# Kernel optimization log

Measured on AMD Instinct MI355X. Metric: run time of the kernel, lower is better.

## Reference

```python
import jax, jax.numpy as jnp
import numpy as np

S, B_BOX, C = 7, 2, 20
LAMBDA_COORD = 5.0
LAMBDA_NOOBJ = 0.5


def _iou(b1, b2):
    # b1, b2: [..., 4] in (cx, cy, w, h) format
    area1 = b1[..., 2] * b1[..., 3]
    area2 = b2[..., 2] * b2[..., 3]
    max_left = jnp.maximum(b1[..., 0] - b1[..., 2] / 2, b2[..., 0] - b2[..., 2] / 2)
    min_right = jnp.minimum(b1[..., 0] + b1[..., 2] / 2, b2[..., 0] + b2[..., 2] / 2)
    max_top = jnp.maximum(b1[..., 1] - b1[..., 3] / 2, b2[..., 1] - b2[..., 3] / 2)
    min_bottom = jnp.minimum(b1[..., 1] + b1[..., 3] / 2, b2[..., 1] + b2[..., 3] / 2)
    iw = jnp.maximum(min_right - max_left, 0.0)
    ih = jnp.maximum(min_bottom - max_top, 0.0)
    inter = iw * ih
    union = area1 + area2 - inter
    return jnp.where(inter > 0.0, inter / union, 0.0)


def setup_inputs() -> dict:
    key = jax.random.key(0)
    k1, k2, k3 = jax.random.split(key, 3)
    batch = 16384
    shape = (batch, S, S, C + 5 * B_BOX)  # [..., 30]
    pred = jax.random.uniform(k1, shape, dtype=jnp.float32)
    target = jax.random.uniform(k2, shape, dtype=jnp.float32)
    # objectness flag must be exactly 1.0 to trigger the obj branch
    obj_flag = jax.random.bernoulli(k3, 0.3, shape[:-1]).astype(jnp.float32)
    target = target.at[..., 0].set(obj_flag)
    return {"pred": pred, "target": target}


def reference(pred, target):
    batch = pred.shape[0]
    pred = pred.reshape(-1, S, S, C + 5 * B_BOX)
    target = target.reshape(-1, S, S, C + 5 * B_BOX)

    obj = (target[..., 0] == 1.0)          # [b,S,S] bool
    obj_f = obj.astype(pred.dtype)
    noobj_f = 1.0 - obj_f

    gt = target[..., 1:5]
    box1 = pred[..., 1:5]                   # predictor 1 box
    box2 = target[..., 6:10]                # NOTE: original code uses target's 2nd box
    iou1 = jax.lax.stop_gradient(_iou(box1, gt))
    iou2 = jax.lax.stop_gradient(_iou(box2, gt))
    resp1 = iou1 > iou2                     # predictor 1 responsible (strict >)
    r1 = resp1[..., None]

    # coord losses (responsible predictor)
    pxy = jnp.where(r1, pred[..., 1:3], pred[..., 6:8])
    txy = jnp.where(r1, target[..., 1:3], target[..., 6:8])
    pwh = jnp.where(r1, pred[..., 3:5], pred[..., 8:10])
    twh = jnp.where(r1, target[..., 3:5], target[..., 8:10])
    cell_xy = jnp.sum((pxy - txy) ** 2, axis=-1)
    cell_wh = jnp.sum((jnp.sqrt(pwh) - jnp.sqrt(twh)) ** 2, axis=-1)

    # obj confidence loss: responsible conf vs its iou
    conf_resp = jnp.where(resp1, pred[..., 0], pred[..., 5])
    iou_resp = jnp.where(resp1, iou1, iou2)
    cell_obj = (conf_resp - iou_resp) ** 2

    # noobj: non-responsible conf in obj cells; both confs in empty cells
    conf_other = jnp.where(resp1, pred[..., 5], pred[..., 0])
    cell_noobj_obj = conf_other ** 2
    cell_noobj_empty = pred[..., 0] ** 2 + pred[..., 5] ** 2

    cell_class = jnp.sum((pred[..., 10:] - target[..., 10:]) ** 2, axis=-1)

    loss_coord_xy = LAMBDA_COORD * jnp.sum(obj_f * cell_xy)
    loss_coord_wh = LAMBDA_COORD * jnp.sum(obj_f * cell_wh)
    loss_obj = jnp.sum(obj_f * cell_obj)
    loss_noobj = LAMBDA_NOOBJ * (jnp.sum(obj_f * cell_noobj_obj) + jnp.sum(noobj_f * cell_noobj_empty))
    loss_class = jnp.sum(obj_f * cell_class)
    loss = loss_coord_xy + loss_coord_wh + loss_obj + loss_noobj + loss_class

    bs = jnp.asarray(batch, pred.dtype)
    return ((loss_coord_xy + loss_coord_wh) / bs,
            loss_obj / bs,
            loss_noobj / bs,
            loss_class / bs,
            loss / bs)
```

## Files before the change

kernel.cpp:

```cpp
#include <hip/hip_runtime.h>

#define NCH 30
#define F2PC 15
#define F4PP 15
#define THREADS 256

typedef float fvec2 __attribute__((ext_vector_type(2)));
typedef float fvec4 __attribute__((ext_vector_type(4)));

__device__ __forceinline__ float iou_fn(float x1, float y1, float w1, float h1,
                                        float x2, float y2, float w2, float h2) {
    float a1 = w1 * h1, a2 = w2 * h2;
    float left  = fmaxf(x1 - w1 * 0.5f, x2 - w2 * 0.5f);
    float right = fminf(x1 + w1 * 0.5f, x2 + w2 * 0.5f);
    float top   = fmaxf(y1 - h1 * 0.5f, y2 - h2 * 0.5f);
    float bot   = fminf(y1 + h1 * 0.5f, y2 + h2 * 0.5f);
    float iw = fmaxf(right - left, 0.0f);
    float ih = fmaxf(bot - top, 0.0f);
    float inter = iw * ih;
    float uni = a1 + a2 - inter;
    return (inter > 0.0f) ? (inter / uni) : 0.0f;
}

__device__ __forceinline__ void cell_losses(const float* p, const float* t,
                                            float& coord, float& lobj,
                                            float& lnoobj, float& lclass) {
    float obj_f = (t[0] == 1.0f) ? 1.0f : 0.0f;

    float iou1 = iou_fn(p[1], p[2], p[3], p[4], t[1], t[2], t[3], t[4]);
    float iou2 = iou_fn(t[6], t[7], t[8], t[9], t[1], t[2], t[3], t[4]);
    bool r = iou1 > iou2;

    float px = r ? p[1] : p[6], py = r ? p[2] : p[7];
    float pw = r ? p[3] : p[8], ph = r ? p[4] : p[9];
    float tx = r ? t[1] : t[6], ty = r ? t[2] : t[7];
    float tw = r ? t[3] : t[8], th = r ? t[4] : t[9];

    float dx = px - tx, dy = py - ty;
    float cxy = dx * dx + dy * dy;
    float swv = sqrtf(pw) - sqrtf(tw), shv = sqrtf(ph) - sqrtf(th);
    float cwh = swv * swv + shv * shv;

    float conf_resp  = r ? p[0] : p[5];
    float iou_resp   = r ? iou1 : iou2;
    float conf_other = r ? p[5] : p[0];
    float dconf = conf_resp - iou_resp;

    coord  += obj_f * (cxy + cwh);
    lobj   += obj_f * dconf * dconf;
    lnoobj += obj_f * conf_other * conf_other
            + (1.0f - obj_f) * (p[0] * p[0] + p[5] * p[5]);

    float cls = 0.0f;
#pragma unroll
    for (int i = 10; i < NCH; i++) { float e = p[i] - t[i]; cls += e * e; }
    lclass += obj_f * cls;
}

__global__ __launch_bounds__(THREADS) void yolo_main(
        const fvec4* __restrict__ pred4, const fvec4* __restrict__ targ4,
        float4* __restrict__ partials, int n_pairs, int n_cells) {
    const int tid = threadIdx.x;
    float coord = 0.f, lobj = 0.f, lnoobj = 0.f, lclass = 0.f;

    for (long long i = (long long)blockIdx.x * THREADS + tid;
         i < n_pairs;
         i += (long long)gridDim.x * THREADS) {
        const long long c0 = 2 * i;
        if (c0 + 1 < (long long)n_cells) {
            float p[2 * NCH], t[2 * NCH];
            const fvec4* pp = pred4 + i * F4PP;
            const fvec4* tp = targ4 + i * F4PP;
#pragma unroll
            for (int k = 0; k < F4PP; k++) {
                fvec4 v = pp[k];
                p[4 * k] = v.x; p[4 * k + 1] = v.y; p[4 * k + 2] = v.z; p[4 * k + 3] = v.w;
            }
#pragma unroll
            for (int k = 0; k < F4PP; k++) {
                fvec4 v = tp[k];
                t[4 * k] = v.x; t[4 * k + 1] = v.y; t[4 * k + 2] = v.z; t[4 * k + 3] = v.w;
            }
            cell_losses(p, t, coord, lobj, lnoobj, lclass);
            cell_losses(p + NCH, t + NCH, coord, lobj, lnoobj, lclass);
        } else if (c0 < (long long)n_cells) {
            float p[NCH], t[NCH];
            const fvec2* pp = reinterpret_cast<const fvec2*>(pred4) + c0 * F2PC;
            const fvec2* tp = reinterpret_cast<const fvec2*>(targ4) + c0 * F2PC;
#pragma unroll
            for (int k = 0; k < F2PC; k++) { fvec2 v = pp[k]; p[2 * k] = v.x; p[2 * k + 1] = v.y; }
#pragma unroll
            for (int k = 0; k < F2PC; k++) { fvec2 v = tp[k]; t[2 * k] = v.x; t[2 * k + 1] = v.y; }
            cell_losses(p, t, coord, lobj, lnoobj, lclass);
        }
    }

#pragma unroll
    for (int off = 32; off > 0; off >>= 1) {
        coord  += __shfl_down(coord, off);
        lobj   += __shfl_down(lobj, off);
        lnoobj += __shfl_down(lnoobj, off);
        lclass += __shfl_down(lclass, off);
    }

    __shared__ float red[4][4];
    int lane = tid & 63;
    int wid  = tid >> 6;
    if (lane == 0) {
        red[wid][0] = coord; red[wid][1] = lobj;
        red[wid][2] = lnoobj; red[wid][3] = lclass;
    }
    __syncthreads();
    if (tid == 0) {
        float s0 = 0.f, s1 = 0.f, s2 = 0.f, s3 = 0.f;
        for (int w = 0; w < 4; w++) {
            s0 += red[w][0]; s1 += red[w][1];
            s2 += red[w][2]; s3 += red[w][3];
        }
        partials[blockIdx.x] = make_float4(s0, s1, s2, s3);
    }
}

__global__ __launch_bounds__(THREADS) void yolo_reduce(
        const float4* __restrict__ partials, int nparts,
        float* __restrict__ out, double inv_bs) {
    double s0 = 0.0, s1 = 0.0, s2 = 0.0, s3 = 0.0;
    for (int i = threadIdx.x; i < nparts; i += THREADS) {
        float4 v = partials[i];
        s0 += (double)v.x; s1 += (double)v.y;
        s2 += (double)v.z; s3 += (double)v.w;
    }
#pragma unroll
    for (int off = 32; off > 0; off >>= 1) {
        s0 += __shfl_down(s0, off);
        s1 += __shfl_down(s1, off);
        s2 += __shfl_down(s2, off);
        s3 += __shfl_down(s3, off);
    }
    __shared__ double red[4][4];
    int lane = threadIdx.x & 63;
    int wid  = threadIdx.x >> 6;
    if (lane == 0) {
        red[wid][0] = s0; red[wid][1] = s1;
        red[wid][2] = s2; red[wid][3] = s3;
    }
    __syncthreads();
    if (threadIdx.x == 0) {
        double a0 = 0, a1 = 0, a2 = 0, a3 = 0;
        for (int w = 0; w < 4; w++) {
            a0 += red[w][0]; a1 += red[w][1];
            a2 += red[w][2]; a3 += red[w][3];
        }
        double cd = a0 * 5.0 * inv_bs;
        double o  = a1 * inv_bs;
        double n  = a2 * 0.5 * inv_bs;
        double cl = a3 * inv_bs;
        out[0] = (float)cd;
        out[1] = (float)o;
        out[2] = (float)n;
        out[3] = (float)cl;
        out[4] = (float)(cd + o + n + cl);
    }
}

extern "C" void kernel_launch(void* const* d_in, const int* in_sizes, int n_in,
                              void* d_out, int out_size, void* d_ws, size_t ws_size,
                              hipStream_t stream) {
    const fvec4* pred4 = (const fvec4*)d_in[0];
    const fvec4* targ4 = (const fvec4*)d_in[1];
    float* out = (float*)d_out;
    float4* partials = (float4*)d_ws;

    int n_cells = in_sizes[0] / NCH;
    int batch   = n_cells / 49;
    int n_pairs = (n_cells + 1) / 2;

    int grid = (n_pairs + THREADS - 1) / THREADS;
    if (grid < 1) grid = 1;

    int max_parts = (int)(ws_size / sizeof(float4));
    if (max_parts >= 1 && grid > max_parts) grid = max_parts;

    yolo_main<<<grid, THREADS, 0, stream>>>(pred4, targ4, partials, n_pairs, n_cells);
    yolo_reduce<<<1, THREADS, 0, stream>>>(partials, grid, out, 1.0 / (double)batch);
}
```

Before: 212.1 us.

## Stage cell tiles through LDS with coalesced loads and register prefetch

Each 64-thread block now loads a 64-cell tile with fully coalesced float4 loads into registers. It writes the tile to LDS, and each thread then reads its own cell from there. This replaces the old strided per-thread float4 loads. The next tile is prefetched into registers while the current one is computed, and the grid is capped so blocks loop persistently. This targets uncoalesced global access; the cost is LDS traffic and bank conflicts from the stride-15 fvec2 reads, plus small one-wave blocks.

```diff
diff --git a/kernel.cpp b/kernel.cpp
--- a/kernel.cpp
+++ b/kernel.cpp
@@ -2,8 +2,9 @@
 
 #define NCH 30
 #define F2PC 15
-#define F4PP 15
-#define THREADS 256
+#define TILE 64
+#define TPB 64
+#define MAXB 2560
 
 typedef float fvec2 __attribute__((ext_vector_type(2)));
 typedef float fvec4 __attribute__((ext_vector_type(4)));
@@ -57,41 +58,81 @@
     lclass += obj_f * cls;
 }
 
-__global__ __launch_bounds__(THREADS) void yolo_main(
-        const fvec4* __restrict__ pred4, const fvec4* __restrict__ targ4,
-        float4* __restrict__ partials, int n_pairs, int n_cells) {
-    const int tid = threadIdx.x;
+__global__ __launch_bounds__(TPB) void yolo_main(
+        const float* __restrict__ pred, const float* __restrict__ targ,
+        float4* __restrict__ partials, int n_full, int n_cells) {
+    __shared__ fvec4 sp4[TILE * F2PC / 2];
+    __shared__ fvec4 st4[TILE * F2PC / 2];
+
+    const int lane = threadIdx.x;
     float coord = 0.f, lobj = 0.f, lnoobj = 0.f, lclass = 0.f;
 
-    for (long long i = (long long)blockIdx.x * THREADS + tid;
-         i < n_pairs;
-         i += (long long)gridDim.x * THREADS) {
-        const long long c0 = 2 * i;
-        if (c0 + 1 < (long long)n_cells) {
-            float p[2 * NCH], t[2 * NCH];
-            const fvec4* pp = pred4 + i * F4PP;
-            const fvec4* tp = targ4 + i * F4PP;
-#pragma unroll
-            for (int k = 0; k < F4PP; k++) {
-                fvec4 v = pp[k];
-                p[4 * k] = v.x; p[4 * k + 1] = v.y; p[4 * k + 2] = v.z; p[4 * k + 3] = v.w;
+    fvec4 rp[7], rt[7];
+    fvec2 rp7, rt7;
+
+    int t = blockIdx.x;
+    bool have = t < n_full;
+    if (have) {
+        const long long b4 = (long long)t * 480;
+#pragma unroll
+        for (int k = 0; k < 7; k++) {
+            rp[k] = reinterpret_cast<const fvec4*>(pred)[b4 + k * 64 + lane];
+            rt[k] = reinterpret_cast<const fvec4*>(targ)[b4 + k * 64 + lane];
+        }
+        rp7 = reinterpret_cast<const fvec2*>(pred)[2 * b4 + 896 + lane];
+        rt7 = reinterpret_cast<const fvec2*>(targ)[2 * b4 + 896 + lane];
+    }
+
+    while (have) {
+        const int tn = t + gridDim.x;
+        const bool have_n = tn < n_full;
+
+        __syncthreads();
+#pragma unroll
+        for (int k = 0; k < 7; k++) {
+            sp4[k * 64 + lane] = rp[k];
+            st4[k * 64 + lane] = rt[k];
+        }
+        reinterpret_cast<fvec2*>(sp4)[896 + lane] = rp7;
+        reinterpret_cast<fvec2*>(st4)[896 + lane] = rt7;
+        __syncthreads();
+
+        if (have_n) {
+            const long long b4 = (long long)tn * 480;
+#pragma unroll
+            for (int k = 0; k < 7; k++) {
+                rp[k] = reinterpret_cast<const fvec4*>(pred)[b4 + k * 64 + lane];
+                rt[k] = reinterpret_cast<const fvec4*>(targ)[b4 + k * 64 + lane];
             }
-#pragma unroll
-            for (int k = 0; k < F4PP; k++) {
-                fvec4 v = tp[k];
-                t[4 * k] = v.x; t[4 * k + 1] = v.y; t[4 * k + 2] = v.z; t[4 * k + 3] = v.w;
-            }
-            cell_losses(p, t, coord, lobj, lnoobj, lclass);
-            cell_losses(p + NCH, t + NCH, coord, lobj, lnoobj, lclass);
-        } else if (c0 < (long long)n_cells) {
-            float p[NCH], t[NCH];
-            const fvec2* pp = reinterpret_cast<const fvec2*>(pred4) + c0 * F2PC;
-            const fvec2* tp = reinterpret_cast<const fvec2*>(targ4) + c0 * F2PC;
+            rp7 = reinterpret_cast<const fvec2*>(pred)[2 * b4 + 896 + lane];
+            rt7 = reinterpret_cast<const fvec2*>(targ)[2 * b4 + 896 + lane];
+        }
+
+        {
+            float p[NCH], tt[NCH];
+            const fvec2* pp = reinterpret_cast<const fvec2*>(sp4) + lane * F2PC;
+            const fvec2* tp = reinterpret_cast<const fvec2*>(st4) + lane * F2PC;
 #pragma unroll
             for (int k = 0; k < F2PC; k++) { fvec2 v = pp[k]; p[2 * k] = v.x; p[2 * k + 1] = v.y; }
 #pragma unroll
-            for (int k = 0; k < F2PC; k++) { fvec2 v = tp[k]; t[2 * k] = v.x; t[2 * k + 1] = v.y; }
-            cell_losses(p, t, coord, lobj, lnoobj, lclass);
+            for (int k = 0; k < F2PC; k++) { fvec2 v = tp[k]; tt[2 * k] = v.x; tt[2 * k + 1] = v.y; }
+            cell_losses(p, tt, coord, lobj, lnoobj, lclass);
+        }
+
+        t = tn; have = have_n;
+    }
+
+    if (blockIdx.x == 0) {
+        int cell = n_full * TILE + lane;
+        if (cell < n_cells) {
+            float p[NCH], tt[NCH];
+            const fvec2* pp = reinterpret_cast<const fvec2*>(pred) + (long long)cell * F2PC;
+            const fvec2* tp = reinterpret_cast<const fvec2*>(targ) + (long long)cell * F2PC;
+#pragma unroll
+            for (int k = 0; k < F2PC; k++) { fvec2 v = pp[k]; p[2 * k] = v.x; p[2 * k + 1] = v.y; }
+#pragma unroll
+            for (int k = 0; k < F2PC; k++) { fvec2 v = tp[k]; tt[2 * k] = v.x; tt[2 * k + 1] = v.y; }
+            cell_losses(p, tt, coord, lobj, lnoobj, lclass);
         }
     }
 
@@ -102,30 +143,14 @@
         lnoobj += __shfl_down(lnoobj, off);
         lclass += __shfl_down(lclass, off);
     }
-
-    __shared__ float red[4][4];
-    int lane = tid & 63;
-    int wid  = tid >> 6;
-    if (lane == 0) {
-        red[wid][0] = coord; red[wid][1] = lobj;
-        red[wid][2] = lnoobj; red[wid][3] = lclass;
-    }
-    __syncthreads();
-    if (tid == 0) {
-        float s0 = 0.f, s1 = 0.f, s2 = 0.f, s3 = 0.f;
-        for (int w = 0; w < 4; w++) {
-            s0 += red[w][0]; s1 += red[w][1];
-            s2 += red[w][2]; s3 += red[w][3];
-        }
-        partials[blockIdx.x] = make_float4(s0, s1, s2, s3);
-    }
-}
-
-__global__ __launch_bounds__(THREADS) void yolo_reduce(
+    if (lane == 0) partials[blockIdx.x] = make_float4(coord, lobj, lnoobj, lclass);
+}
+
+__global__ __launch_bounds__(256) void yolo_reduce(
         const float4* __restrict__ partials, int nparts,
         float* __restrict__ out, double inv_bs) {
     double s0 = 0.0, s1 = 0.0, s2 = 0.0, s3 = 0.0;
-    for (int i = threadIdx.x; i < nparts; i += THREADS) {
+    for (int i = threadIdx.x; i < nparts; i += 256) {
         float4 v = partials[i];
         s0 += (double)v.x; s1 += (double)v.y;
         s2 += (double)v.z; s3 += (double)v.w;
@@ -166,21 +191,20 @@
 extern "C" void kernel_launch(void* const* d_in, const int* in_sizes, int n_in,
                               void* d_out, int out_size, void* d_ws, size_t ws_size,
                               hipStream_t stream) {
-    const fvec4* pred4 = (const fvec4*)d_in[0];
-    const fvec4* targ4 = (const fvec4*)d_in[1];
+    const float* pred = (const float*)d_in[0];
+    const float* targ = (const float*)d_in[1];
     float* out = (float*)d_out;
     float4* partials = (float4*)d_ws;
 
     int n_cells = in_sizes[0] / NCH;
     int batch   = n_cells / 49;
-    int n_pairs = (n_cells + 1) / 2;
-
-    int grid = (n_pairs + THREADS - 1) / THREADS;
-    if (grid < 1) grid = 1;
+    int n_full  = n_cells / TILE;
+
+    int grid = (n_full < 1) ? 1 : (n_full < MAXB ? n_full : MAXB);
 
     int max_parts = (int)(ws_size / sizeof(float4));
     if (max_parts >= 1 && grid > max_parts) grid = max_parts;
 
-    yolo_main<<<grid, THREADS, 0, stream>>>(pred4, targ4, partials, n_pairs, n_cells);
-    yolo_reduce<<<1, THREADS, 0, stream>>>(partials, grid, out, 1.0 / (double)batch);
-}
+    yolo_main<<<grid, TPB, 0, stream>>>(pred, targ, partials, n_full, n_cells);
+    yolo_reduce<<<1, 256, 0, stream>>>(partials, grid, out, 1.0 / (double)batch);
+}
```

Result: no change. 210.6 us (-0.7%).
